# Kernel optimization log

Measured on AMD Instinct MI355X. Metric: run time of the kernel, lower is better.

## Reference

```python
import jax, jax.numpy as jnp
import numpy as np

N_NODES = 50000
N_EDGES = 800000
IN_DIM = 128
HIDDEN = 64
HEADS = 4
OUT_DIM = 32
NEG_SLOPE = 0.2  # PyG GATConv default negative_slope


def _glorot(key, shape):
    fan = shape[0] + shape[-1]
    return jax.random.normal(key, shape, dtype=jnp.float32) * jnp.sqrt(2.0 / fan)


def setup_inputs() -> dict:
    key = jax.random.key(0)
    ks = jax.random.split(key, 8)
    x = jax.random.normal(ks[0], (N_NODES, IN_DIM), dtype=jnp.float32)
    edge_index = jax.random.randint(ks[1], (2, N_EDGES), 0, N_NODES, dtype=jnp.int64)
    return {
        "x": x,
        "edge_index": edge_index,
        "W1": _glorot(ks[2], (IN_DIM, HEADS * HIDDEN)),
        "a_src1": _glorot(ks[3], (HEADS, HIDDEN)),
        "a_dst1": _glorot(ks[4], (HEADS, HIDDEN)),
        "b1": jnp.zeros((HEADS * HIDDEN,), dtype=jnp.float32),
        "W2": _glorot(ks[5], (HEADS * HIDDEN, OUT_DIM)),
        "a_src2": _glorot(ks[6], (1, OUT_DIM)),
        "a_dst2": _glorot(ks[7], (1, OUT_DIM)),
        "b2": jnp.zeros((OUT_DIM,), dtype=jnp.float32),
    }


def gat_conv(x, src, dst, W, a_src, a_dst, b, heads, feat, concat):
    """PyG-style GATConv (self-loops already appended to src/dst)."""
    n = x.shape[0]
    h = (x @ W).reshape(n, heads, feat)              # [N, H, F]
    alpha_s = jnp.einsum("nhf,hf->nh", h, a_src)     # [N, H]
    alpha_d = jnp.einsum("nhf,hf->nh", h, a_dst)     # [N, H]
    logits = jax.nn.leaky_relu(alpha_s[src] + alpha_d[dst], NEG_SLOPE)  # [E, H]
    # segment softmax over edges grouped by destination node
    seg_max = jax.ops.segment_max(logits, dst, num_segments=n)          # [N, H]
    expd = jnp.exp(logits - seg_max[dst])
    seg_sum = jax.ops.segment_sum(expd, dst, num_segments=n)            # [N, H]
    alpha = expd / (seg_sum[dst] + 1e-16)                               # [E, H]
    # scatter-aggregate weighted messages from source nodes
    out = jax.ops.segment_sum(h[src] * alpha[:, :, None], dst, num_segments=n)  # [N, H, F]
    out = out.reshape(n, heads * feat) if concat else out.mean(axis=1)
    return out + b


def reference(x, edge_index, W1, a_src1, a_dst1, b1, W2, a_src2, a_dst2, b2):
    n = x.shape[0]
    loop = jnp.arange(n, dtype=edge_index.dtype)
    src = jnp.concatenate([edge_index[0], loop])  # add_self_loops=True (PyG default)
    dst = jnp.concatenate([edge_index[1], loop])
    h = jax.nn.elu(gat_conv(x, src, dst, W1, a_src1, a_dst1, b1, HEADS, HIDDEN, True))
    return gat_conv(h, src, dst, W2, a_src2, a_dst2, b2, 1, OUT_DIM, False)
```

## Files before the change

### kernel.cpp

```cpp
#include <hip/hip_runtime.h>
#include <hip/hip_bf16.h>

#define N_NODES 50000
#define N_EDGES 800000
#define E_TOT   850000
#define IN_DIM  128
#define C1      256
#define HEADS   4
#define HID     64
#define OUT_DIM 32
#define NEG_SLOPE 0.2f
#define SCAN_NBLK 196

typedef __attribute__((ext_vector_type(8))) short bf16x8;
typedef __attribute__((ext_vector_type(8))) unsigned short u16x8;
typedef __attribute__((ext_vector_type(4))) float f32x4;

__device__ __forceinline__ void edge_sd(const int* __restrict__ ei, int e, int& s, int& d) {
    if (e < N_EDGES) { s = ei[e]; d = ei[N_EDGES + e]; }
    else             { s = d = e - N_EDGES; }
}

__device__ __forceinline__ unsigned short f2bf(float f) {
    unsigned u = __float_as_uint(f);
    u += 0x7fffu + ((u >> 16) & 1u);
    return (unsigned short)(u >> 16);
}
__device__ __forceinline__ float bf2f(unsigned short u) {
    return __uint_as_float(((unsigned)u) << 16);
}
__device__ __forceinline__ float4 bf4_to_f4(ushort4 v) {
    return make_float4(bf2f(v.x), bf2f(v.y), bf2f(v.z), bf2f(v.w));
}

__global__ __launch_bounds__(256) void setup_kernel(const float* __restrict__ W1,
                                                    const float* __restrict__ W2,
                                                    unsigned short* __restrict__ Bp1,
                                                    unsigned short* __restrict__ Bp2,
                                                    int* __restrict__ deg) {
    int tid = blockIdx.x * 256 + threadIdx.x;
    if (tid < N_NODES) deg[tid] = 0;
    if (tid < IN_DIM * C1) {
        int j = tid & 7, q = (tid >> 3) & 3, n = (tid >> 5) & 255, K0 = tid >> 13;
        int k = K0 * 32 + q * 8 + j;
        Bp1[tid] = f2bf(W1[k * C1 + n]);
        if (tid < C1 * OUT_DIM) {
            int j2 = tid & 7, q2 = (tid >> 3) & 3, n2 = (tid >> 5) & 31, K02 = tid >> 10;
            int k2 = K02 * 32 + q2 * 8 + j2;
            Bp2[tid] = f2bf(W2[k2 * OUT_DIM + n2]);
        }
    }
}

__global__ __launch_bounds__(256) void deg_kernel(const int* __restrict__ ei,
                                                  int* __restrict__ deg,
                                                  int* __restrict__ pos) {
    int e = blockIdx.x * 256 + threadIdx.x;
    if (e >= E_TOT) return;
    int s, d; edge_sd(ei, e, s, d);
    pos[e] = atomicAdd(&deg[d], 1);
}

__global__ __launch_bounds__(256) void scanA_kernel(const int* __restrict__ deg,
                                                    int* __restrict__ incl,
                                                    int* __restrict__ blocksum) {
    __shared__ int sm[256];
    int t = threadIdx.x, idx = blockIdx.x * 256 + t;
    int v = (idx < N_NODES) ? deg[idx] : 0;
    sm[t] = v; __syncthreads();
#pragma unroll
    for (int off = 1; off < 256; off <<= 1) {
        int u = (t >= off) ? sm[t - off] : 0;
        __syncthreads();
        sm[t] += u;
        __syncthreads();
    }
    if (idx < N_NODES) incl[idx] = sm[t];
    if (t == 255) blocksum[blockIdx.x] = sm[t];
}

__global__ __launch_bounds__(256) void scanC_kernel(const int* __restrict__ deg,
                                                    const int* __restrict__ incl,
                                                    const int* __restrict__ blocksum,
                                                    int* __restrict__ row_start) {
    __shared__ int wsum[4];
    int t = threadIdx.x;
    int v = (t < (int)blockIdx.x) ? blocksum[t] : 0;
#pragma unroll
    for (int m = 32; m >= 1; m >>= 1) v += __shfl_xor(v, m, 64);
    if ((t & 63) == 0) wsum[t >> 6] = v;
    __syncthreads();
    int off = wsum[0] + wsum[1] + wsum[2] + wsum[3];
    int idx = blockIdx.x * 256 + t;
    if (idx >= N_NODES) return;
    row_start[idx] = off + incl[idx] - deg[idx];
    if (idx == N_NODES - 1) row_start[N_NODES] = off + incl[idx];
}

__global__ __launch_bounds__(256) void scatter_w_kernel(const int* __restrict__ ei,
                                                        const int* __restrict__ row_start,
                                                        const int* __restrict__ pos,
                                                        const float* __restrict__ as1,
                                                        const float* __restrict__ ad1,
                                                        int* __restrict__ csr_src,
                                                        float* __restrict__ wc) {
    int e = blockIdx.x * 256 + threadIdx.x;
    if (e >= E_TOT) return;
    int s, d; edge_sd(ei, e, s, d);
    int p = row_start[d] + pos[e];
    csr_src[p] = s;
    float4 av = *(const float4*)&as1[s * 4];
    float4 bv = *(const float4*)&ad1[d * 4];
    float l0 = av.x + bv.x, l1 = av.y + bv.y, l2 = av.z + bv.z, l3 = av.w + bv.w;
    l0 = l0 > 0.f ? l0 : NEG_SLOPE * l0;
    l1 = l1 > 0.f ? l1 : NEG_SLOPE * l1;
    l2 = l2 > 0.f ? l2 : NEG_SLOPE * l2;
    l3 = l3 > 0.f ? l3 : NEG_SLOPE * l3;
    *(float4*)&wc[(size_t)p * 4] =
        make_float4(__expf(l0), __expf(l1), __expf(l2), __expf(l3));
}

__global__ __launch_bounds__(256) void gemm1_kernel(const float* __restrict__ x,
                                                    const unsigned short* __restrict__ Bp,
                                                    const float* __restrict__ a_src1,
                                                    const float* __restrict__ a_dst1,
                                                    unsigned short* __restrict__ h1b,
                                                    float* __restrict__ as1,
                                                    float* __restrict__ ad1) {
    __shared__ unsigned short xs[16][136];
    const int t = threadIdx.x;
    const int row0 = blockIdx.x * 16;
    {
        int r = t >> 4, k0 = (t & 15) * 8;
        const float* xp = &x[(size_t)(row0 + r) * IN_DIM + k0];
        float4 v0 = *(const float4*)xp;
        float4 v1 = *(const float4*)(xp + 4);
        ushort4 o0, o1;
        o0.x = f2bf(v0.x); o0.y = f2bf(v0.y); o0.z = f2bf(v0.z); o0.w = f2bf(v0.w);
        o1.x = f2bf(v1.x); o1.y = f2bf(v1.y); o1.z = f2bf(v1.z); o1.w = f2bf(v1.w);
        *(ushort4*)&xs[r][k0] = o0;
        *(ushort4*)&xs[r][k0 + 4] = o1;
    }
    __syncthreads();
    const int wave = t >> 6;
    const int lane = t & 63;
    const int nl = lane & 15, q = lane >> 4;
    f32x4 acc[4];
    f32x4 z = {0.f, 0.f, 0.f, 0.f};
    acc[0] = z; acc[1] = z; acc[2] = z; acc[3] = z;
#pragma unroll
    for (int K0 = 0; K0 < 4; ++K0) {
        bf16x8 af = *(const bf16x8*)&xs[nl][K0 * 32 + q * 8];
#pragma unroll
        for (int sub = 0; sub < 4; ++sub) {
            int n = wave * 64 + sub * 16 + nl;
            bf16x8 bfv = *(const bf16x8*)&Bp[((size_t)(K0 * 256 + n) * 4 + q) * 8];
            acc[sub] = __builtin_amdgcn_mfma_f32_16x16x32_bf16(af, bfv, acc[sub], 0, 0, 0);
        }
    }
    float asv[4], adv[4];
#pragma unroll
    for (int sub = 0; sub < 4; ++sub) {
        asv[sub] = a_src1[wave * 64 + sub * 16 + nl];
        adv[sub] = a_dst1[wave * 64 + sub * 16 + nl];
    }
#pragma unroll
    for (int r = 0; r < 4; ++r) {
        int gr = row0 + q * 4 + r;
        float ps = 0.f, pd = 0.f;
#pragma unroll
        for (int sub = 0; sub < 4; ++sub) {
            float v = acc[sub][r];
            h1b[(size_t)gr * C1 + wave * 64 + sub * 16 + nl] = f2bf(v);
            ps += v * asv[sub];
            pd += v * adv[sub];
        }
#pragma unroll
        for (int m = 8; m >= 1; m >>= 1) {
            ps += __shfl_xor(ps, m, 16);
            pd += __shfl_xor(pd, m, 16);
        }
        if (nl == 0) {
            as1[gr * 4 + wave] = ps;
            ad1[gr * 4 + wave] = pd;
        }
    }
}

__global__ __launch_bounds__(256) void agg1_kernel(const int* __restrict__ csr_src,
                                                   const int* __restrict__ row_start,
                                                   const unsigned short* __restrict__ h1b,
                                                   const float* __restrict__ wc,
                                                   const float* __restrict__ b1,
                                                   unsigned short* __restrict__ hpb) {
    int n = (blockIdx.x * 256 + threadIdx.x) >> 6;
    if (n >= N_NODES) return;
    int lane = threadIdx.x & 63;
    int h = lane >> 4;
    int beg = __builtin_amdgcn_readfirstlane(row_start[n]);
    int end = __builtin_amdgcn_readfirstlane(row_start[n + 1]);
    float4 acc = make_float4(0.f, 0.f, 0.f, 0.f);
    float sumw = 0.f;
    int i = beg;
    for (; i + 8 <= end; i += 8) {
        int s[8];
#pragma unroll
        for (int u = 0; u < 8; ++u) s[u] = __builtin_amdgcn_readfirstlane(csr_src[i + u]);
        float w[8];
#pragma unroll
        for (int u = 0; u < 8; ++u) w[u] = wc[(size_t)(i + u) * 4 + h];
        ushort4 rv[8];
#pragma unroll
        for (int u = 0; u < 8; ++u) rv[u] = *(const ushort4*)&h1b[(size_t)s[u] * C1 + lane * 4];
#pragma unroll
        for (int u = 0; u < 8; ++u) {
            sumw += w[u];
            float4 f = bf4_to_f4(rv[u]);
            acc.x += w[u] * f.x; acc.y += w[u] * f.y;
            acc.z += w[u] * f.z; acc.w += w[u] * f.w;
        }
    }
    if (i < end) {
        int s[8]; int ic[8]; bool va[8];
#pragma unroll
        for (int u = 0; u < 8; ++u) {
            va[u] = (i + u) < end;
            ic[u] = va[u] ? i + u : beg;
            s[u] = __builtin_amdgcn_readfirstlane(csr_src[ic[u]]);
        }
        float w[8];
#pragma unroll
        for (int u = 0; u < 8; ++u) w[u] = va[u] ? wc[(size_t)ic[u] * 4 + h] : 0.f;
        ushort4 rv[8];
#pragma unroll
        for (int u = 0; u < 8; ++u) rv[u] = *(const ushort4*)&h1b[(size_t)s[u] * C1 + lane * 4];
#pragma unroll
        for (int u = 0; u < 8; ++u) {
            sumw += w[u];
            float4 f = bf4_to_f4(rv[u]);
            acc.x += w[u] * f.x; acc.y += w[u] * f.y;
            acc.z += w[u] * f.z; acc.w += w[u] * f.w;
        }
    }
    float inv = 1.f / (sumw + 1e-16f);
    const float4 bv = *(const float4*)&b1[lane * 4];
    float v0 = acc.x * inv + bv.x;
    float v1 = acc.y * inv + bv.y;
    float v2 = acc.z * inv + bv.z;
    float v3 = acc.w * inv + bv.w;
    v0 = v0 > 0.f ? v0 : __expf(v0) - 1.f;
    v1 = v1 > 0.f ? v1 : __expf(v1) - 1.f;
    v2 = v2 > 0.f ? v2 : __expf(v2) - 1.f;
    v3 = v3 > 0.f ? v3 : __expf(v3) - 1.f;
    ushort4 o;
    o.x = f2bf(v0); o.y = f2bf(v1); o.z = f2bf(v2); o.w = f2bf(v3);
    *(ushort4*)&hpb[(size_t)n * C1 + lane * 4] = o;
}

__global__ __launch_bounds__(256) void gemm2_kernel(const unsigned short* __restrict__ hpb,
                                                    const unsigned short* __restrict__ Bp2,
                                                    const float* __restrict__ a_src2,
                                                    const float* __restrict__ a_dst2,
                                                    unsigned short* __restrict__ h2b,
                                                    float* __restrict__ as2,
                                                    float* __restrict__ ad2) {
    __shared__ unsigned short xs[64][264];
    const int t = threadIdx.x;
    const int row0 = blockIdx.x * 64;
    for (int idx = t; idx < 2048; idx += 256) {
        int r = idx >> 5, ch = (idx & 31) * 8;
        int gr = row0 + r;
        u16x8 v = {0, 0, 0, 0, 0, 0, 0, 0};
        if (gr < N_NODES) v = *(const u16x8*)&hpb[(size_t)gr * C1 + ch];
        *(u16x8*)&xs[r][ch] = v;
    }
    __syncthreads();
    const int wave = t >> 6, lane = t & 63;
    const int nl = lane & 15, q = lane >> 4;
    f32x4 acc0 = {0.f, 0.f, 0.f, 0.f}, acc1 = {0.f, 0.f, 0.f, 0.f};
#pragma unroll
    for (int K0 = 0; K0 < 8; ++K0) {
        bf16x8 af = *(const bf16x8*)&xs[wave * 16 + nl][K0 * 32 + q * 8];
        bf16x8 b0 = *(const bf16x8*)&Bp2[((size_t)(K0 * 32 + nl) * 4 + q) * 8];
        bf16x8 b1v = *(const bf16x8*)&Bp2[((size_t)(K0 * 32 + 16 + nl) * 4 + q) * 8];
        acc0 = __builtin_amdgcn_mfma_f32_16x16x32_bf16(af, b0, acc0, 0, 0, 0);
        acc1 = __builtin_amdgcn_mfma_f32_16x16x32_bf16(af, b1v, acc1, 0, 0, 0);
    }
    float a_s0 = a_src2[nl], a_s1 = a_src2[16 + nl];
    float a_d0 = a_dst2[nl], a_d1 = a_dst2[16 + nl];
#pragma unroll
    for (int r = 0; r < 4; ++r) {
        int gr = row0 + wave * 16 + q * 4 + r;
        if (gr < N_NODES) {
            h2b[(size_t)gr * OUT_DIM + nl] = f2bf(acc0[r]);
            h2b[(size_t)gr * OUT_DIM + 16 + nl] = f2bf(acc1[r]);
            float ps = acc0[r] * a_s0 + acc1[r] * a_s1;
            float pd = acc0[r] * a_d0 + acc1[r] * a_d1;
#pragma unroll
            for (int m = 8; m >= 1; m >>= 1) {
                ps += __shfl_xor(ps, m, 16);
                pd += __shfl_xor(pd, m, 16);
            }
            if (nl == 0) { as2[gr] = ps; ad2[gr] = pd; }
        }
    }
}

__global__ __launch_bounds__(256) void agg2_kernel(const int* __restrict__ csr_src,
                                                   const int* __restrict__ row_start,
                                                   const unsigned short* __restrict__ h2b,
                                                   const float* __restrict__ as2,
                                                   const float* __restrict__ ad2,
                                                   const float* __restrict__ b2,
                                                   float* __restrict__ out) {
    int n = (blockIdx.x * 256 + threadIdx.x) >> 6;
    if (n >= N_NODES) return;
    int lane = threadIdx.x & 63;
    int g  = lane >> 3;
    int c4 = lane & 7;
    int beg = __builtin_amdgcn_readfirstlane(row_start[n]);
    int end = __builtin_amdgcn_readfirstlane(row_start[n + 1]);
    float ad = ad2[n];
    float4 acc = make_float4(0.f, 0.f, 0.f, 0.f);
    float sumw = 0.f;
    for (int i = beg; i < end; i += 8) {
        int idx = i + g;
        bool valid = idx < end;
        int ic = valid ? idx : beg;
        int s = csr_src[ic];
        float l = as2[s] + ad;
        l = l > 0.f ? l : NEG_SLOPE * l;
        float w = valid ? __expf(l) : 0.f;
        sumw += w;
        float4 hv = bf4_to_f4(*(const ushort4*)&h2b[(size_t)s * OUT_DIM + c4 * 4]);
        acc.x += w * hv.x; acc.y += w * hv.y; acc.z += w * hv.z; acc.w += w * hv.w;
    }
#pragma unroll
    for (int m = 8; m <= 32; m <<= 1) {
        sumw  += __shfl_xor(sumw, m, 64);
        acc.x += __shfl_xor(acc.x, m, 64);
        acc.y += __shfl_xor(acc.y, m, 64);
        acc.z += __shfl_xor(acc.z, m, 64);
        acc.w += __shfl_xor(acc.w, m, 64);
    }
    if (g == 0) {
        float inv = 1.f / (sumw + 1e-16f);
        const float4 bv = *(const float4*)&b2[c4 * 4];
        *(float4*)&out[(size_t)n * OUT_DIM + c4 * 4] =
            make_float4(acc.x * inv + bv.x, acc.y * inv + bv.y,
                        acc.z * inv + bv.z, acc.w * inv + bv.w);
    }
}

extern "C" void kernel_launch(void* const* d_in, const int* in_sizes, int n_in,
                              void* d_out, int out_size, void* d_ws, size_t ws_size,
                              hipStream_t stream) {
    const float* x      = (const float*)d_in[0];
    const int*   ei     = (const int*)d_in[1];
    const float* W1     = (const float*)d_in[2];
    const float* a_src1 = (const float*)d_in[3];
    const float* a_dst1 = (const float*)d_in[4];
    const float* b1     = (const float*)d_in[5];
    const float* W2     = (const float*)d_in[6];
    const float* a_src2 = (const float*)d_in[7];
    const float* a_dst2 = (const float*)d_in[8];
    const float* b2     = (const float*)d_in[9];
    float* out = (float*)d_out;

    unsigned short* h1b = (unsigned short*)d_ws;
    unsigned short* hpb = h1b + 12800000;
    unsigned short* h2b = hpb + 12800000;
    unsigned short* Bp1 = h2b + 1600000;
    unsigned short* Bp2 = Bp1 + 32768;
    float* as1    = (float*)(Bp2 + 8192);
    float* ad1    = as1 + 200000;
    float* as2    = ad1 + 200000;
    float* ad2    = as2 + 50000;
    float* wc     = ad2 + 50000;
    int* csr_src  = (int*)(wc + (size_t)E_TOT * 4);
    int* row_start= csr_src + E_TOT;
    int* deg      = row_start + (N_NODES + 1);
    int* pos      = deg + N_NODES;
    int* incl     = pos + E_TOT;
    int* blocksum = incl + N_NODES;

    const int EB = (E_TOT + 255) / 256;
    setup_kernel<<<SCAN_NBLK, 256, 0, stream>>>(W1, W2, Bp1, Bp2, deg);
    deg_kernel<<<EB, 256, 0, stream>>>(ei, deg, pos);
    scanA_kernel<<<SCAN_NBLK, 256, 0, stream>>>(deg, incl, blocksum);
    scanC_kernel<<<SCAN_NBLK, 256, 0, stream>>>(deg, incl, blocksum, row_start);

    gemm1_kernel<<<N_NODES / 16, 256, 0, stream>>>(x, Bp1, a_src1, a_dst1, h1b, as1, ad1);
    scatter_w_kernel<<<EB, 256, 0, stream>>>(ei, row_start, pos, as1, ad1, csr_src, wc);
    agg1_kernel<<<(N_NODES * 64 + 255) / 256, 256, 0, stream>>>(csr_src, row_start, h1b, wc, b1, hpb);

    gemm2_kernel<<<(N_NODES + 63) / 64, 256, 0, stream>>>(hpb, Bp2, a_src2, a_dst2, h2b, as2, ad2);
    agg2_kernel<<<(N_NODES * 64 + 255) / 256, 256, 0, stream>>>(csr_src, row_start, h2b, as2, ad2, b2, out);
}
```

Baseline: 272.9 us.

## Interleave edge weights and source ids into 32-byte CSR records, unroll aggregation deeper

Packs the four per-head softmax weights and the source index of each CSR edge into one 32-byte record, replacing the separate csr_src and wc arrays. The scatter kernel then writes a single record per edge. agg1 now processes 16 edges per main-loop iteration to keep more gathers in flight, and agg2 handles two 8-edge groups per loop iteration. The cost is more record bytes for agg2, which only needs the source id and now strides 32 bytes per edge, plus extra register pressure in agg1 from the wider unroll.

```diff
diff --git a/kernel.cpp b/kernel.cpp
--- a/kernel.cpp
+++ b/kernel.cpp
@@ -102,13 +102,11 @@
                                                         const int* __restrict__ pos,
                                                         const float* __restrict__ as1,
                                                         const float* __restrict__ ad1,
-                                                        int* __restrict__ csr_src,
-                                                        float* __restrict__ wc) {
+                                                        float* __restrict__ rec) {
     int e = blockIdx.x * 256 + threadIdx.x;
     if (e >= E_TOT) return;
     int s, d; edge_sd(ei, e, s, d);
-    int p = row_start[d] + pos[e];
-    csr_src[p] = s;
+    size_t p = (size_t)(row_start[d] + pos[e]) * 8;
     float4 av = *(const float4*)&as1[s * 4];
     float4 bv = *(const float4*)&ad1[d * 4];
     float l0 = av.x + bv.x, l1 = av.y + bv.y, l2 = av.z + bv.z, l3 = av.w + bv.w;
@@ -116,8 +114,8 @@
     l1 = l1 > 0.f ? l1 : NEG_SLOPE * l1;
     l2 = l2 > 0.f ? l2 : NEG_SLOPE * l2;
     l3 = l3 > 0.f ? l3 : NEG_SLOPE * l3;
-    *(float4*)&wc[(size_t)p * 4] =
-        make_float4(__expf(l0), __expf(l1), __expf(l2), __expf(l3));
+    *(float4*)&rec[p] = make_float4(__expf(l0), __expf(l1), __expf(l2), __expf(l3));
+    ((int*)rec)[p + 4] = s;
 }
 
 __global__ __launch_bounds__(256) void gemm1_kernel(const float* __restrict__ x,
@@ -187,28 +185,46 @@
     }
 }
 
-__global__ __launch_bounds__(256) void agg1_kernel(const int* __restrict__ csr_src,
+__global__ __launch_bounds__(256) void agg1_kernel(const float* __restrict__ rec,
                                                    const int* __restrict__ row_start,
                                                    const unsigned short* __restrict__ h1b,
-                                                   const float* __restrict__ wc,
                                                    const float* __restrict__ b1,
                                                    unsigned short* __restrict__ hpb) {
     int n = (blockIdx.x * 256 + threadIdx.x) >> 6;
     if (n >= N_NODES) return;
     int lane = threadIdx.x & 63;
     int h = lane >> 4;
+    const int* reci = (const int*)rec;
     int beg = __builtin_amdgcn_readfirstlane(row_start[n]);
     int end = __builtin_amdgcn_readfirstlane(row_start[n + 1]);
     float4 acc = make_float4(0.f, 0.f, 0.f, 0.f);
     float sumw = 0.f;
     int i = beg;
-    for (; i + 8 <= end; i += 8) {
-        int s[8];
-#pragma unroll
-        for (int u = 0; u < 8; ++u) s[u] = __builtin_amdgcn_readfirstlane(csr_src[i + u]);
-        float w[8];
-#pragma unroll
-        for (int u = 0; u < 8; ++u) w[u] = wc[(size_t)(i + u) * 4 + h];
+    for (; i + 16 <= end; i += 16) {
+        int s[16]; float w[16];
+#pragma unroll
+        for (int u = 0; u < 16; ++u) {
+            s[u] = __builtin_amdgcn_readfirstlane(reci[(size_t)(i + u) * 8 + 4]);
+            w[u] = rec[(size_t)(i + u) * 8 + h];
+        }
+        ushort4 rv[16];
+#pragma unroll
+        for (int u = 0; u < 16; ++u) rv[u] = *(const ushort4*)&h1b[(size_t)s[u] * C1 + lane * 4];
+#pragma unroll
+        for (int u = 0; u < 16; ++u) {
+            sumw += w[u];
+            float4 f = bf4_to_f4(rv[u]);
+            acc.x += w[u] * f.x; acc.y += w[u] * f.y;
+            acc.z += w[u] * f.z; acc.w += w[u] * f.w;
+        }
+    }
+    if (i + 8 <= end) {
+        int s[8]; float w[8];
+#pragma unroll
+        for (int u = 0; u < 8; ++u) {
+            s[u] = __builtin_amdgcn_readfirstlane(reci[(size_t)(i + u) * 8 + 4]);
+            w[u] = rec[(size_t)(i + u) * 8 + h];
+        }
         ushort4 rv[8];
 #pragma unroll
         for (int u = 0; u < 8; ++u) rv[u] = *(const ushort4*)&h1b[(size_t)s[u] * C1 + lane * 4];
@@ -219,18 +235,17 @@
             acc.x += w[u] * f.x; acc.y += w[u] * f.y;
             acc.z += w[u] * f.z; acc.w += w[u] * f.w;
         }
+        i += 8;
     }
     if (i < end) {
-        int s[8]; int ic[8]; bool va[8];
+        int s[8]; float w[8];
 #pragma unroll
         for (int u = 0; u < 8; ++u) {
-            va[u] = (i + u) < end;
-            ic[u] = va[u] ? i + u : beg;
-            s[u] = __builtin_amdgcn_readfirstlane(csr_src[ic[u]]);
-        }
-        float w[8];
-#pragma unroll
-        for (int u = 0; u < 8; ++u) w[u] = va[u] ? wc[(size_t)ic[u] * 4 + h] : 0.f;
+            bool va = (i + u) < end;
+            int ic = va ? i + u : beg;
+            s[u] = __builtin_amdgcn_readfirstlane(reci[(size_t)ic * 8 + 4]);
+            w[u] = va ? rec[(size_t)ic * 8 + h] : 0.f;
+        }
         ushort4 rv[8];
 #pragma unroll
         for (int u = 0; u < 8; ++u) rv[u] = *(const ushort4*)&h1b[(size_t)s[u] * C1 + lane * 4];
@@ -306,7 +321,7 @@
     }
 }
 
-__global__ __launch_bounds__(256) void agg2_kernel(const int* __restrict__ csr_src,
+__global__ __launch_bounds__(256) void agg2_kernel(const float* __restrict__ rec,
                                                    const int* __restrict__ row_start,
                                                    const unsigned short* __restrict__ h2b,
                                                    const float* __restrict__ as2,
@@ -318,22 +333,26 @@
     int lane = threadIdx.x & 63;
     int g  = lane >> 3;
     int c4 = lane & 7;
+    const int* reci = (const int*)rec;
     int beg = __builtin_amdgcn_readfirstlane(row_start[n]);
     int end = __builtin_amdgcn_readfirstlane(row_start[n + 1]);
     float ad = ad2[n];
     float4 acc = make_float4(0.f, 0.f, 0.f, 0.f);
     float sumw = 0.f;
-    for (int i = beg; i < end; i += 8) {
-        int idx = i + g;
-        bool valid = idx < end;
-        int ic = valid ? idx : beg;
-        int s = csr_src[ic];
-        float l = as2[s] + ad;
-        l = l > 0.f ? l : NEG_SLOPE * l;
-        float w = valid ? __expf(l) : 0.f;
-        sumw += w;
-        float4 hv = bf4_to_f4(*(const ushort4*)&h2b[(size_t)s * OUT_DIM + c4 * 4]);
-        acc.x += w * hv.x; acc.y += w * hv.y; acc.z += w * hv.z; acc.w += w * hv.w;
+    for (int i = beg; i < end; i += 16) {
+#pragma unroll
+        for (int b = 0; b < 2; ++b) {
+            int idx = i + b * 8 + g;
+            bool valid = idx < end;
+            int ic = valid ? idx : beg;
+            int s = reci[(size_t)ic * 8 + 4];
+            float l = as2[s] + ad;
+            l = l > 0.f ? l : NEG_SLOPE * l;
+            float w = valid ? __expf(l) : 0.f;
+            sumw += w;
+            float4 hv = bf4_to_f4(*(const ushort4*)&h2b[(size_t)s * OUT_DIM + c4 * 4]);
+            acc.x += w * hv.x; acc.y += w * hv.y; acc.z += w * hv.z; acc.w += w * hv.w;
+        }
     }
 #pragma unroll
     for (int m = 8; m <= 32; m <<= 1) {
@@ -376,9 +395,8 @@
     float* ad1    = as1 + 200000;
     float* as2    = ad1 + 200000;
     float* ad2    = as2 + 50000;
-    float* wc     = ad2 + 50000;
-    int* csr_src  = (int*)(wc + (size_t)E_TOT * 4);
-    int* row_start= csr_src + E_TOT;
+    float* rec    = ad2 + 50000;
+    int* row_start= (int*)(rec + (size_t)E_TOT * 8);
     int* deg      = row_start + (N_NODES + 1);
     int* pos      = deg + N_NODES;
     int* incl     = pos + E_TOT;
@@ -391,9 +409,9 @@
     scanC_kernel<<<SCAN_NBLK, 256, 0, stream>>>(deg, incl, blocksum, row_start);
 
     gemm1_kernel<<<N_NODES / 16, 256, 0, stream>>>(x, Bp1, a_src1, a_dst1, h1b, as1, ad1);
-    scatter_w_kernel<<<EB, 256, 0, stream>>>(ei, row_start, pos, as1, ad1, csr_src, wc);
-    agg1_kernel<<<(N_NODES * 64 + 255) / 256, 256, 0, stream>>>(csr_src, row_start, h1b, wc, b1, hpb);
+    scatter_w_kernel<<<EB, 256, 0, stream>>>(ei, row_start, pos, as1, ad1, rec);
+    agg1_kernel<<<(N_NODES * 64 + 255) / 256, 256, 0, stream>>>(rec, row_start, h1b, b1, hpb);
 
     gemm2_kernel<<<(N_NODES + 63) / 64, 256, 0, stream>>>(hpb, Bp2, a_src2, a_dst2, h2b, as2, ad2);
-    agg2_kernel<<<(N_NODES * 64 + 255) / 256, 256, 0, stream>>>(csr_src, row_start, h2b, as2, ad2, b2, out);
-}
+    agg2_kernel<<<(N_NODES * 64 + 255) / 256, 256, 0, stream>>>(rec, row_start, h2b, as2, ad2, b2, out);
+}
```

Result: no change. 271.5 us (-0.5%).
